# Performance work log

Hardware: AMD Instinct MI355X
Metric: run time of the kernel (lower is better)

## Reference

```python
import jax, jax.numpy as jnp
import numpy as np

B, N, M, D, H = 8, 2048, 2048, 512, 8


def setup_inputs() -> dict:
    key = jax.random.key(0)
    ks = jax.random.split(key, 12)
    std = D ** (-0.5)
    inp = {
        "k": jax.random.normal(ks[0], (B, N, D), jnp.float32),
        "v": jax.random.normal(ks[1], (B, N, D), jnp.float32),
        "q": jax.random.normal(ks[2], (B, M, D), jnp.float32),
        # per-head projections, stacked over the head axis: [H, D, D]
        "Wk": jax.random.normal(ks[3], (H, D, D), jnp.float32) * std,
        "bk": jax.random.normal(ks[4], (H, D), jnp.float32) * 0.01,
        "Wv": jax.random.normal(ks[5], (H, D, D), jnp.float32) * std,
        "bv": jax.random.normal(ks[6], (H, D), jnp.float32) * 0.01,
        "Wq": jax.random.normal(ks[7], (H, D, D), jnp.float32) * std,
        "bq": jax.random.normal(ks[8], (H, D), jnp.float32) * 0.01,
        # final linear: input ordering is (hidden_dim, head) flattened -> H*D
        "Wo": jax.random.normal(ks[9], (H * D, D), jnp.float32) * (H * D) ** (-0.5),
        "bo": jax.random.normal(ks[10], (D,), jnp.float32) * 0.01,
    }
    return inp


def reference(k, v, q, Wk, bk, Wv, bv, Wq, bq, Wo, bo):
    # Per-head linear projections (torch loops over heads; here batched over h).
    # nn.Linear computes x @ W.T + b; Wk here stores W.T directly as [H, D, D].
    k_ = jnp.einsum("bnd,hde->bhne", k, Wk) + bk[None, :, None, :]  # [B,H,N,D]
    v_ = jnp.einsum("bnd,hde->bhne", v, Wv) + bv[None, :, None, :]  # [B,H,N,D]
    q_ = jnp.einsum("bmd,hde->bhme", q, Wq) + bq[None, :, None, :]  # [B,H,M,D]

    scale = D ** 0.5
    scores = jnp.einsum("bhmd,bhnd->bhmn", q_, k_) / scale  # [B,H,M,N]
    weights = jax.nn.softmax(scores, axis=-1)
    out = jnp.einsum("bhmn,bhnd->bhmd", weights, v_)  # [B,H,M,D]

    # torch: stack(outs, dim=-1) -> [B,M,D,H], then view -> [B,M,D*H]
    outs = jnp.transpose(out, (0, 2, 3, 1)).reshape(B, M, D * H)
    # matching flatten order (d-major, h-minor) requires Wo rows ordered d*H+h;
    # setup generates Wo random so any consistent ordering is faithful.
    rep = outs @ Wo + bo  # [B,M,D]
    return rep
```

## Files before the change

### kernel.cpp

```cpp
#include <hip/hip_runtime.h>
#include <hip/hip_bf16.h>
#include <cstdint>
#include <cstddef>

typedef __bf16 bf16x8 __attribute__((ext_vector_type(8)));
typedef __bf16 bf16x4 __attribute__((ext_vector_type(4)));
typedef float floatx4 __attribute__((ext_vector_type(4)));

#define MFMA16(a, b, c) __builtin_amdgcn_mfma_f32_16x16x32_bf16((a), (b), (c), 0, 0, 0)

__device__ __forceinline__ void load_lds16(const __bf16* g, __bf16* l) {
  __builtin_amdgcn_global_load_lds(
      (const __attribute__((address_space(1))) uint32_t*)(g),
      (__attribute__((address_space(3))) uint32_t*)(l), 16, 0, 0);
}

#define BAR_LGKM()                                        \
  do {                                                    \
    asm volatile("s_waitcnt lgkmcnt(0)" ::: "memory");    \
    __builtin_amdgcn_s_barrier();                         \
    __builtin_amdgcn_sched_barrier(0);                    \
  } while (0)

__device__ __forceinline__ int xcd_swizzle(int orig, int nwg) {
  int q = nwg >> 3, r = nwg & 7;
  int xcd = orig & 7, local = orig >> 3;
  return (xcd < r) ? xcd * (q + 1) + local : r * (q + 1) + (xcd - r) * q + local;
}

__global__ __launch_bounds__(256) void tw_t(const float* __restrict__ W,
                                            __bf16* __restrict__ Wt, float scale) {
  __shared__ float tile[64][65];
  int h = blockIdx.z, d0 = blockIdx.y * 64, e0 = blockIdx.x * 64;
  int tx = threadIdx.x & 15, ty = threadIdx.x >> 4;
  const float* src = W + ((size_t)h * 512 + d0) * 512 + e0;
#pragma unroll
  for (int j = 0; j < 4; ++j) {
    int dd = ty + j * 16;
    float4 f = *(const float4*)&src[(size_t)dd * 512 + tx * 4];
    tile[dd][tx * 4 + 0] = f.x; tile[dd][tx * 4 + 1] = f.y;
    tile[dd][tx * 4 + 2] = f.z; tile[dd][tx * 4 + 3] = f.w;
  }
  __syncthreads();
  __bf16* dst = Wt + ((size_t)h * 512 + e0) * 512 + d0;
#pragma unroll
  for (int j = 0; j < 4; ++j) {
    int ee = ty + j * 16;
    bf16x4 v;
#pragma unroll
    for (int x = 0; x < 4; ++x) v[x] = (__bf16)(tile[tx * 4 + x][ee] * scale);
    *(bf16x4*)&dst[(size_t)ee * 512 + tx * 4] = v;
  }
}

__global__ __launch_bounds__(256) void wo_t(const float* __restrict__ Wo,
                                            __bf16* __restrict__ Wot) {
  __shared__ float tile[64][65];
  int h = blockIdx.z, d0 = blockIdx.y * 64, e0 = blockIdx.x * 64;
  int tx = threadIdx.x & 15, ty = threadIdx.x >> 4;
#pragma unroll
  for (int j = 0; j < 4; ++j) {
    int dd = ty + j * 16;
    float4 f = *(const float4*)&Wo[(size_t)((d0 + dd) * 8 + h) * 512 + e0 + tx * 4];
    tile[dd][tx * 4 + 0] = f.x; tile[dd][tx * 4 + 1] = f.y;
    tile[dd][tx * 4 + 2] = f.z; tile[dd][tx * 4 + 3] = f.w;
  }
  __syncthreads();
#pragma unroll
  for (int j = 0; j < 4; ++j) {
    int ee = ty + j * 16;
    bf16x4 v;
#pragma unroll
    for (int x = 0; x < 4; ++x) v[x] = (__bf16)tile[tx * 4 + x][ee];
    *(bf16x4*)&Wot[(size_t)(e0 + ee) * 4096 + h * 512 + d0 + tx * 4] = v;
  }
}

__global__ __launch_bounds__(256) void cvt_bf16(const float* __restrict__ in,
                                                __bf16* __restrict__ out, int n8) {
  int i = blockIdx.x * 256 + threadIdx.x;
  if (i < n8) {
    float4 f0 = *(const float4*)&in[(size_t)i * 8];
    float4 f1 = *(const float4*)&in[(size_t)i * 8 + 4];
    bf16x8 v;
    v[0] = (__bf16)f0.x; v[1] = (__bf16)f0.y; v[2] = (__bf16)f0.z; v[3] = (__bf16)f0.w;
    v[4] = (__bf16)f1.x; v[5] = (__bf16)f1.y; v[6] = (__bf16)f1.z; v[7] = (__bf16)f1.w;
    *(bf16x8*)&out[(size_t)i * 8] = v;
  }
}

template <int EPI>
__global__ __launch_bounds__(256) void gemm_bt(const __bf16* __restrict__ A,
                                               const __bf16* __restrict__ Bt,
                                               const float* __restrict__ bias,
                                               void* __restrict__ Cout,
                                               int N, int K, float bscale) {
  __shared__ __align__(16) __bf16 sA[128 * 64];
  __shared__ __align__(16) __bf16 sB[128 * 64];
  const int tid = threadIdx.x;
  const int lane = tid & 63;
  const int wave = tid >> 6;
  const int lr = lane & 15;
  const int lq = lane >> 4;
  const int wm = (wave >> 1) * 64;
  const int wn = (wave & 1) * 64;
  const int bx = blockIdx.x, by = blockIdx.y;

  const floatx4 z4 = {0.f, 0.f, 0.f, 0.f};
  floatx4 acc[4][4];
#pragma unroll
  for (int i = 0; i < 4; ++i)
#pragma unroll
    for (int j = 0; j < 4; ++j) acc[i][j] = z4;

  const size_t abase = (size_t)(by * 128) * K;
  const size_t bbase = (size_t)(bx * 128) * K;
  const int col8 = (tid & 7) << 3;

  for (int k0 = 0; k0 < K; k0 += 64) {
#pragma unroll
    for (int p = 0; p < 4; ++p) {
      int row = (p * 256 + tid) >> 3;
      load_lds16(&A[abase + (size_t)row * K + k0 + col8], &sA[p * 2048 + wave * 512]);
      load_lds16(&Bt[bbase + (size_t)row * K + k0 + col8], &sB[p * 2048 + wave * 512]);
    }
    __syncthreads();
#pragma unroll
    for (int ks = 0; ks < 2; ++ks) {
      bf16x8 af[4], bfr[4];
#pragma unroll
      for (int mt = 0; mt < 4; ++mt)
        af[mt] = *(const bf16x8*)&sA[(wm + mt * 16 + lr) * 64 + ks * 32 + lq * 8];
#pragma unroll
      for (int nt = 0; nt < 4; ++nt)
        bfr[nt] = *(const bf16x8*)&sB[(wn + nt * 16 + lr) * 64 + ks * 32 + lq * 8];
#pragma unroll
      for (int mt = 0; mt < 4; ++mt)
#pragma unroll
        for (int nt = 0; nt < 4; ++nt) acc[mt][nt] = MFMA16(af[mt], bfr[nt], acc[mt][nt]);
    }
    __syncthreads();
  }

#pragma unroll
  for (int mt = 0; mt < 4; ++mt) {
#pragma unroll
    for (int nt = 0; nt < 4; ++nt) {
      int col = bx * 128 + wn + nt * 16 + lr;
      int row0 = by * 128 + wm + mt * 16 + lq * 4;
      float bcol = bias[col] * bscale;
      if (EPI == 0) {
        __bf16* dst = (__bf16*)Cout;
        int h = col >> 9, e = col & 511;
#pragma unroll
        for (int r = 0; r < 4; ++r) {
          int row = row0 + r;
          int b = row >> 11, m = row & 2047;
          dst[((size_t)((b << 3) | h) * 2048 + m) * 512 + e] = (__bf16)(acc[mt][nt][r] + bcol);
        }
      } else if (EPI == 1) {
        __bf16* dst = (__bf16*)Cout;
        int h = col >> 9, e = col & 511;
        int b = row0 >> 11, n = row0 & 2047;
        bf16x4 pk;
#pragma unroll
        for (int r = 0; r < 4; ++r) pk[r] = (__bf16)(acc[mt][nt][r] + bcol);
        *(bf16x4*)&dst[((size_t)((b << 3) | h) * 512 + e) * 2048 + n] = pk;
      } else {
        float* dst = (float*)Cout;
#pragma unroll
        for (int r = 0; r < 4; ++r) {
          int row = row0 + r;
          dst[(size_t)row * N + col] = acc[mt][nt][r] + bcol;
        }
      }
    }
  }
}

__global__ __launch_bounds__(512, 2) void attn_kernel(const __bf16* __restrict__ Qp,
                                                      const __bf16* __restrict__ Kp,
                                                      const __bf16* __restrict__ Vt,
                                                      __bf16* __restrict__ Outs) {
  __shared__ __align__(16) __bf16 kls[2][32 * 512];
  __shared__ __align__(16) __bf16 vls[2][512 * 32];
  __shared__ __align__(16) __bf16 pls[128 * 40];
  __shared__ __align__(16) floatx4 sx[2][8][64];
  __shared__ __align__(16) float l_red[128];
  const int tid = threadIdx.x;
  const int lane = tid & 63;
  const int wave = tid >> 6;
  const int lr = lane & 15;
  const int lq = lane >> 4;
  const int blk = xcd_swizzle(blockIdx.x, gridDim.x);
  const int bh = blk >> 4;
  const int mblk = blk & 15;
  const int rp = (wave & 3) * 2;
  const int dh = wave >> 2;
  const int fg = rp + dh;
  const int e0 = wave * 64;
  const int mbase = mblk * 128;
  const __bf16* Qb = Qp + (size_t)bh * (2048 * 512);
  const __bf16* Kb = Kp + (size_t)bh * (2048 * 512);
  const __bf16* Vb = Vt + (size_t)bh * (512 * 2048);

  int gK[4], gV[4];
#pragma unroll
  for (int i = 0; i < 4; ++i) {
    int q = i * 512 + tid;
    int rK = q >> 6;
    gK[i] = rK * 512 + ((q & 63) ^ (rK & 7)) * 8;
    int eV = q >> 2;
    gV[i] = eV * 2048 + ((q & 3) ^ (eV & 3)) * 8;
  }

  bf16x8 qf[2][8];
#pragma unroll
  for (int ks = 0; ks < 8; ++ks) {
    qf[0][ks] = *(const bf16x8*)&Qb[(size_t)(mbase + fg * 16 + lr) * 512 +
                                    dh * 256 + ks * 32 + lq * 8];
    qf[1][ks] = *(const bf16x8*)&Qb[(size_t)(mbase + (rp + (dh ^ 1)) * 16 + lr) * 512 +
                                    dh * 256 + ks * 32 + lq * 8];
  }

  const floatx4 z4 = {0.f, 0.f, 0.f, 0.f};
  floatx4 o[8][4];
#pragma unroll
  for (int mt = 0; mt < 8; ++mt)
#pragma unroll
    for (int et = 0; et < 4; ++et) o[mt][et] = z4;
  float lsum[4] = {0.f, 0.f, 0.f, 0.f};

#pragma unroll
  for (int i = 0; i < 4; ++i) {
    load_lds16(Kb + gK[i], &kls[0][i * 4096 + wave * 512]);
    load_lds16(Vb + gV[i], &vls[0][i * 4096 + wave * 512]);
  }
  __syncthreads();

  for (int t = 0; t < 64; ++t) {
    const int cur = t & 1;
    if (t < 63) {
      const __bf16* kg = Kb + (size_t)(t + 1) * (32 * 512);
      const __bf16* vg = Vb + (t + 1) * 32;
#pragma unroll
      for (int i = 0; i < 4; ++i) {
        load_lds16(kg + gK[i], &kls[cur ^ 1][i * 4096 + wave * 512]);
        load_lds16(vg + gV[i], &vls[cur ^ 1][i * 4096 + wave * 512]);
      }
    }
    floatx4 sm0 = z4, sm1 = z4, sp0 = z4, sp1 = z4;
    const __bf16* kc = kls[cur];
    __builtin_amdgcn_s_setprio(1);
#pragma unroll
    for (int ks = 0; ks < 8; ++ks) {
      int cidx = ((dh * 32 + ks * 4 + lq) ^ (lr & 7)) * 8;
      bf16x8 k0 = *(const bf16x8*)&kc[lr * 512 + cidx];
      bf16x8 k1 = *(const bf16x8*)&kc[(16 + lr) * 512 + cidx];
      sm0 = MFMA16(qf[0][ks], k0, sm0);
      sm1 = MFMA16(qf[0][ks], k1, sm1);
      sp0 = MFMA16(qf[1][ks], k0, sp0);
      sp1 = MFMA16(qf[1][ks], k1, sp1);
    }
    __builtin_amdgcn_s_setprio(0);
    sx[0][wave][lane] = sp0;
    sx[1][wave][lane] = sp1;
    BAR_LGKM();
    {
      floatx4 q0 = sx[0][wave ^ 4][lane];
      floatx4 q1 = sx[1][wave ^ 4][lane];
#pragma unroll
      for (int r = 0; r < 4; ++r) {
        float p0 = __expf(sm0[r] + q0[r]);
        float p1 = __expf(sm1[r] + q1[r]);
        lsum[r] += p0 + p1;
        pls[(fg * 16 + lq * 4 + r) * 40 + lr] = (__bf16)p0;
        pls[(fg * 16 + lq * 4 + r) * 40 + 16 + lr] = (__bf16)p1;
      }
    }
    BAR_LGKM();
    {
      const __bf16* vc = vls[cur];
      bf16x8 vf[4];
#pragma unroll
      for (int et = 0; et < 4; ++et) {
        int e = e0 + et * 16 + lr;
        vf[et] = *(const bf16x8*)&vc[e * 32 + ((lq ^ (e & 3)) * 8)];
      }
      __builtin_amdgcn_s_setprio(1);
#pragma unroll
      for (int mt = 0; mt < 8; ++mt) {
        bf16x8 pf = *(const bf16x8*)&pls[(mt * 16 + lr) * 40 + lq * 8];
#pragma unroll
        for (int et = 0; et < 4; ++et) o[mt][et] = MFMA16(pf, vf[et], o[mt][et]);
      }
      __builtin_amdgcn_s_setprio(0);
    }
    __syncthreads();
  }

#pragma unroll
  for (int r = 0; r < 4; ++r) {
    float s = lsum[r];
    s += __shfl_xor(s, 1);
    s += __shfl_xor(s, 2);
    s += __shfl_xor(s, 4);
    s += __shfl_xor(s, 8);
    lsum[r] = s;
  }
  if (lr == 0) {
#pragma unroll
    for (int r = 0; r < 4; ++r) l_red[fg * 16 + lq * 4 + r] = lsum[r];
  }
  __syncthreads();

  int b = bh >> 3, h = bh & 7;
#pragma unroll
  for (int mt = 0; mt < 8; ++mt) {
    float4 lv = *(const float4*)&l_red[mt * 16 + lq * 4];
    float invr[4] = {1.0f / lv.x, 1.0f / lv.y, 1.0f / lv.z, 1.0f / lv.w};
    size_t rowbase = ((size_t)b * 2048 + mbase + mt * 16 + lq * 4) * 4096 + h * 512 + e0;
#pragma unroll
    for (int et = 0; et < 4; ++et)
#pragma unroll
      for (int r = 0; r < 4; ++r)
        Outs[rowbase + (size_t)r * 4096 + et * 16 + lr] = (__bf16)(o[mt][et][r] * invr[r]);
  }
}

extern "C" void kernel_launch(void* const* d_in, const int* in_sizes, int n_in,
                              void* d_out, int out_size, void* d_ws, size_t ws_size,
                              hipStream_t stream) {
  (void)in_sizes; (void)n_in; (void)out_size;
  const float* kin = (const float*)d_in[0];
  const float* vin = (const float*)d_in[1];
  const float* qin = (const float*)d_in[2];
  const float* Wk  = (const float*)d_in[3];
  const float* bk  = (const float*)d_in[4];
  const float* Wv  = (const float*)d_in[5];
  const float* bv  = (const float*)d_in[6];
  const float* Wq  = (const float*)d_in[7];
  const float* bq  = (const float*)d_in[8];
  const float* Wo  = (const float*)d_in[9];
  const float* bo  = (const float*)d_in[10];
  float* out = (float*)d_out;
  char* ws = (char*)d_ws;

  const float scale = 0.044194173824159216f;

  const size_t SZ_W = (size_t)4096 * 512 * 2;
  const size_t SZ_B = (size_t)8 * 2048 * 512 * 2;
  const size_t FIXED = 4 * SZ_W;

  int nb = 1;
  if (ws_size >= FIXED + 8 * 4 * SZ_B) nb = 8;
  else if (ws_size >= FIXED + 4 * 4 * SZ_B) nb = 4;
  else if (ws_size >= FIXED + 2 * 4 * SZ_B) nb = 2;

  __bf16* Wkt = (__bf16*)(ws);
  __bf16* Wvt = (__bf16*)(ws + SZ_W);
  __bf16* Wqt = (__bf16*)(ws + 2 * SZ_W);
  __bf16* Wot = (__bf16*)(ws + 3 * SZ_W);
  char* chunkbase = ws + FIXED;
  __bf16* kproj = (__bf16*)(chunkbase);
  __bf16* qproj = (__bf16*)(chunkbase + (size_t)nb * SZ_B);
  __bf16* vt    = (__bf16*)(chunkbase + (size_t)nb * 2 * SZ_B);
  __bf16* outs  = (__bf16*)(chunkbase + (size_t)nb * 3 * SZ_B);

  tw_t<<<dim3(8, 8, 8), dim3(256), 0, stream>>>(Wk, Wkt, 1.0f);
  tw_t<<<dim3(8, 8, 8), dim3(256), 0, stream>>>(Wv, Wvt, 1.0f);
  tw_t<<<dim3(8, 8, 8), dim3(256), 0, stream>>>(Wq, Wqt, scale);
  wo_t<<<dim3(8, 8, 8), dim3(256), 0, stream>>>(Wo, Wot);

  for (int b0 = 0; b0 < 8; b0 += nb) {
    const float* kc = kin + (size_t)b0 * 2048 * 512;
    const float* vc = vin + (size_t)b0 * 2048 * 512;
    const float* qc = qin + (size_t)b0 * 2048 * 512;
    const size_t chunk_els = (size_t)nb * 2048 * 512;
    __bf16* kb16 = outs;
    __bf16* qb16 = outs + chunk_els;
    __bf16* vb16 = outs + 2 * chunk_els;
    int n8 = (int)(chunk_els / 8);
    int cvgrid = (n8 + 255) / 256;
    cvt_bf16<<<dim3(cvgrid), dim3(256), 0, stream>>>(kc, kb16, n8);
    cvt_bf16<<<dim3(cvgrid), dim3(256), 0, stream>>>(qc, qb16, n8);
    cvt_bf16<<<dim3(cvgrid), dim3(256), 0, stream>>>(vc, vb16, n8);
    gemm_bt<0><<<dim3(32, nb * 16), dim3(256), 0, stream>>>(kb16, Wkt, bk, (void*)kproj, 4096, 512, 1.0f);
    gemm_bt<0><<<dim3(32, nb * 16), dim3(256), 0, stream>>>(qb16, Wqt, bq, (void*)qproj, 4096, 512, scale);
    gemm_bt<1><<<dim3(32, nb * 16), dim3(256), 0, stream>>>(vb16, Wvt, bv, (void*)vt, 4096, 512, 1.0f);
    attn_kernel<<<dim3(nb * 128), dim3(512), 0, stream>>>(qproj, kproj, vt, outs);
    gemm_bt<2><<<dim3(4, nb * 16), dim3(256), 0, stream>>>(
        outs, Wot, bo, (void*)(out + (size_t)b0 * 2048 * 512), 512, 4096, 1.0f);
  }
}
```

Baseline: 1.645 ms.

## Merge input conversions, pad GEMM LDS tiles, drop attention setprio hints

The three fp32-to-bf16 conversion launches become one launch, with grid.y choosing which of k, q or v to convert, which removes two kernel launches per chunk. The projection GEMM stops using direct global-to-LDS loads and instead does register-staged vector loads into padded 128x72 LDS tiles, aiming to cut bank conflicts on the fragment reads. In exchange the loads now pass through VGPRs and the asynchronous LDS DMA path is lost. The attention kernel also drops its s_setprio raises around the MFMA loops.

```diff
diff --git a/kernel.cpp b/kernel.cpp
--- a/kernel.cpp
+++ b/kernel.cpp
@@ -76,17 +76,23 @@
   }
 }
 
-__global__ __launch_bounds__(256) void cvt_bf16(const float* __restrict__ in,
-                                                __bf16* __restrict__ out, int n8) {
+__global__ __launch_bounds__(256) void cvt_bf16x3(const float* __restrict__ in0,
+                                                  const float* __restrict__ in1,
+                                                  const float* __restrict__ in2,
+                                                  __bf16* __restrict__ out0,
+                                                  __bf16* __restrict__ out1,
+                                                  __bf16* __restrict__ out2,
+                                                  int n8) {
   int i = blockIdx.x * 256 + threadIdx.x;
-  if (i < n8) {
-    float4 f0 = *(const float4*)&in[(size_t)i * 8];
-    float4 f1 = *(const float4*)&in[(size_t)i * 8 + 4];
-    bf16x8 v;
-    v[0] = (__bf16)f0.x; v[1] = (__bf16)f0.y; v[2] = (__bf16)f0.z; v[3] = (__bf16)f0.w;
-    v[4] = (__bf16)f1.x; v[5] = (__bf16)f1.y; v[6] = (__bf16)f1.z; v[7] = (__bf16)f1.w;
-    *(bf16x8*)&out[(size_t)i * 8] = v;
-  }
+  if (i >= n8) return;
+  const float* in = (blockIdx.y == 0) ? in0 : (blockIdx.y == 1) ? in1 : in2;
+  __bf16* out = (blockIdx.y == 0) ? out0 : (blockIdx.y == 1) ? out1 : out2;
+  float4 f0 = *(const float4*)&in[(size_t)i * 8];
+  float4 f1 = *(const float4*)&in[(size_t)i * 8 + 4];
+  bf16x8 v;
+  v[0] = (__bf16)f0.x; v[1] = (__bf16)f0.y; v[2] = (__bf16)f0.z; v[3] = (__bf16)f0.w;
+  v[4] = (__bf16)f1.x; v[5] = (__bf16)f1.y; v[6] = (__bf16)f1.z; v[7] = (__bf16)f1.w;
+  *(bf16x8*)&out[(size_t)i * 8] = v;
 }
 
 template <int EPI>
@@ -95,8 +101,8 @@
                                                const float* __restrict__ bias,
                                                void* __restrict__ Cout,
                                                int N, int K, float bscale) {
-  __shared__ __align__(16) __bf16 sA[128 * 64];
-  __shared__ __align__(16) __bf16 sB[128 * 64];
+  __shared__ __align__(16) __bf16 sA[128][72];
+  __shared__ __align__(16) __bf16 sB[128][72];
   const int tid = threadIdx.x;
   const int lane = tid & 63;
   const int wave = tid >> 6;
@@ -105,6 +111,8 @@
   const int wm = (wave >> 1) * 64;
   const int wn = (wave & 1) * 64;
   const int bx = blockIdx.x, by = blockIdx.y;
+  const int srow = tid >> 3;
+  const int scol = (tid & 7) << 3;
 
   const floatx4 z4 = {0.f, 0.f, 0.f, 0.f};
   floatx4 acc[4][4];
@@ -115,14 +123,13 @@
 
   const size_t abase = (size_t)(by * 128) * K;
   const size_t bbase = (size_t)(bx * 128) * K;
-  const int col8 = (tid & 7) << 3;
 
   for (int k0 = 0; k0 < K; k0 += 64) {
 #pragma unroll
     for (int p = 0; p < 4; ++p) {
-      int row = (p * 256 + tid) >> 3;
-      load_lds16(&A[abase + (size_t)row * K + k0 + col8], &sA[p * 2048 + wave * 512]);
-      load_lds16(&Bt[bbase + (size_t)row * K + k0 + col8], &sB[p * 2048 + wave * 512]);
+      int row = p * 32 + srow;
+      *(bf16x8*)&sA[row][scol] = *(const bf16x8*)&A[abase + (size_t)row * K + k0 + scol];
+      *(bf16x8*)&sB[row][scol] = *(const bf16x8*)&Bt[bbase + (size_t)row * K + k0 + scol];
     }
     __syncthreads();
 #pragma unroll
@@ -130,10 +137,10 @@
       bf16x8 af[4], bfr[4];
 #pragma unroll
       for (int mt = 0; mt < 4; ++mt)
-        af[mt] = *(const bf16x8*)&sA[(wm + mt * 16 + lr) * 64 + ks * 32 + lq * 8];
+        af[mt] = *(const bf16x8*)&sA[wm + mt * 16 + lr][ks * 32 + lq * 8];
 #pragma unroll
       for (int nt = 0; nt < 4; ++nt)
-        bfr[nt] = *(const bf16x8*)&sB[(wn + nt * 16 + lr) * 64 + ks * 32 + lq * 8];
+        bfr[nt] = *(const bf16x8*)&sB[wn + nt * 16 + lr][ks * 32 + lq * 8];
 #pragma unroll
       for (int mt = 0; mt < 4; ++mt)
 #pragma unroll
@@ -251,7 +258,6 @@
     }
     floatx4 sm0 = z4, sm1 = z4, sp0 = z4, sp1 = z4;
     const __bf16* kc = kls[cur];
-    __builtin_amdgcn_s_setprio(1);
 #pragma unroll
     for (int ks = 0; ks < 8; ++ks) {
       int cidx = ((dh * 32 + ks * 4 + lq) ^ (lr & 7)) * 8;
@@ -262,7 +268,6 @@
       sp0 = MFMA16(qf[1][ks], k0, sp0);
       sp1 = MFMA16(qf[1][ks], k1, sp1);
     }
-    __builtin_amdgcn_s_setprio(0);
     sx[0][wave][lane] = sp0;
     sx[1][wave][lane] = sp1;
     BAR_LGKM();
@@ -287,14 +292,12 @@
         int e = e0 + et * 16 + lr;
         vf[et] = *(const bf16x8*)&vc[e * 32 + ((lq ^ (e & 3)) * 8)];
       }
-      __builtin_amdgcn_s_setprio(1);
 #pragma unroll
       for (int mt = 0; mt < 8; ++mt) {
         bf16x8 pf = *(const bf16x8*)&pls[(mt * 16 + lr) * 40 + lq * 8];
 #pragma unroll
         for (int et = 0; et < 4; ++et) o[mt][et] = MFMA16(pf, vf[et], o[mt][et]);
       }
-      __builtin_amdgcn_s_setprio(0);
     }
     __syncthreads();
   }
@@ -382,9 +385,7 @@
     __bf16* vb16 = outs + 2 * chunk_els;
     int n8 = (int)(chunk_els / 8);
     int cvgrid = (n8 + 255) / 256;
-    cvt_bf16<<<dim3(cvgrid), dim3(256), 0, stream>>>(kc, kb16, n8);
-    cvt_bf16<<<dim3(cvgrid), dim3(256), 0, stream>>>(qc, qb16, n8);
-    cvt_bf16<<<dim3(cvgrid), dim3(256), 0, stream>>>(vc, vb16, n8);
+    cvt_bf16x3<<<dim3(cvgrid, 3), dim3(256), 0, stream>>>(kc, qc, vc, kb16, qb16, vb16, n8);
     gemm_bt<0><<<dim3(32, nb * 16), dim3(256), 0, stream>>>(kb16, Wkt, bk, (void*)kproj, 4096, 512, 1.0f);
     gemm_bt<0><<<dim3(32, nb * 16), dim3(256), 0, stream>>>(qb16, Wqt, bq, (void*)qproj, 4096, 512, scale);
     gemm_bt<1><<<dim3(32, nb * 16), dim3(256), 0, stream>>>(vb16, Wvt, bv, (void*)vt, 4096, 512, 1.0f);
```

Measured after the change: 1.526 ms. 1.08x faster.
